# Kernel optimization log

Hardware: AMD Instinct MI355X
Metric: run time of the kernel (lower is better)

Reference implementation:

```python
import jax, jax.numpy as jnp
import numpy as np

D_MODEL = 1024


def setup_inputs() -> dict:
    key = jax.random.key(0)
    kx, kq, kk, kv = jax.random.split(key, 4)
    x = jax.random.normal(kx, (4, 2048, D_MODEL), dtype=jnp.float32)
    s = 1.0 / np.sqrt(D_MODEL)
    # torch nn.Linear weight is [out, in]; y = x @ W.T
    Wq = jax.random.normal(kq, (D_MODEL, D_MODEL), dtype=jnp.float32) * s
    Wk = jax.random.normal(kk, (D_MODEL, D_MODEL), dtype=jnp.float32) * s
    Wv = jax.random.normal(kv, (D_MODEL, D_MODEL), dtype=jnp.float32) * s
    return {"x": x, "Wq": Wq, "Wk": Wk, "Wv": Wv}


def reference(x, Wq, Wk, Wv):
    # Linear projections (no bias): [b, s, d]
    Q = jnp.einsum("bsd,ed->bse", x, Wq)
    K = jnp.einsum("bsd,ed->bse", x, Wk)
    V = jnp.einsum("bsd,ed->bse", x, Wv)
    d_k = Q.shape[-1]
    scores = jnp.einsum("bqd,bkd->bqk", Q, K) / jnp.sqrt(jnp.asarray(d_k, Q.dtype))
    weights = jax.nn.softmax(scores, axis=-1)
    return jnp.einsum("bqk,bkd->bqd", weights, V)
```

## Files before the change

### kernel.cpp

```cpp
#include <hip/hip_runtime.h>
#include <hip/hip_bf16.h>

using bf16 = __hip_bfloat16;
typedef __attribute__((ext_vector_type(8))) short short8;
typedef __attribute__((ext_vector_type(16))) float f32x16;

__global__ __launch_bounds__(256) void cast_all(const float* __restrict__ x,
                                                const float* __restrict__ Wq,
                                                const float* __restrict__ Wk,
                                                const float* __restrict__ Wv,
                                                bf16* __restrict__ xb, bf16* __restrict__ Wb) {
  const int r0 = blockIdx.x << 2;
  const float* src;
  bf16* dst;
  if (r0 < 8192) {
    src = x + (size_t)r0 * 1024;
    dst = xb + (size_t)r0 * 1024;
  } else if (r0 < 9216) {
    src = Wq + (size_t)(r0 - 8192) * 1024;
    dst = Wb + (size_t)(r0 - 8192) * 1024;
  } else if (r0 < 10240) {
    src = Wk + (size_t)(r0 - 9216) * 1024;
    dst = Wb + (size_t)(r0 - 8192) * 1024;
  } else {
    src = Wv + (size_t)(r0 - 10240) * 1024;
    dst = Wb + (size_t)(r0 - 8192) * 1024;
  }
  const int i = threadIdx.x * 16;
#pragma unroll
  for (int q = 0; q < 4; ++q) {
    const float4 f = *(const float4*)(src + i + q * 4);
    bf16 h[4];
    h[0] = __float2bfloat16(f.x);
    h[1] = __float2bfloat16(f.y);
    h[2] = __float2bfloat16(f.z);
    h[3] = __float2bfloat16(f.w);
    *(uint2*)(dst + i + q * 4) = *(const uint2*)h;
  }
}

template <int BN, class Epi>
__device__ __forceinline__ void gemm_nt(const bf16* __restrict__ A, const bf16* __restrict__ B,
                                        int lda, int ldb, int K, int m0, int n0, Epi epi) {
  constexpr int THREADS = BN * 2;
  constexpr int NA = 8192 / (THREADS * 16);
  constexpr int NB = (BN * 64) / (THREADS * 16);
  constexpr int L = NA + NB;
  constexpr int SLOT = (128 + BN) * 64;
  __shared__ char smem[3 * SLOT];
  const int t = threadIdx.x;
  const int lane = t & 63;
  const int wave = t >> 6;
  const int wm = (BN == 256) ? (wave >> 2) * 64 : (wave >> 1) * 64;
  const int wn = (BN == 256) ? (wave & 3) * 64 : (wave & 1) * 64;
  const int rl = lane & 31;
  const int grp = lane >> 5;

  f32x16 acc[2][2];
#pragma unroll
  for (int i = 0; i < 2; ++i)
#pragma unroll
    for (int j = 0; j < 2; ++j)
#pragma unroll
      for (int r = 0; r < 16; ++r) acc[i][j][r] = 0.f;

  const bf16* gA[NA];
#pragma unroll
  for (int j = 0; j < NA; ++j) {
    const int s = j * THREADS + t;
    const int row = s >> 2;
    const int f = (row + (row >> 2)) & 3;
    gA[j] = A + (size_t)(m0 + row) * lda + ((((s & 3) ^ f)) << 3);
  }
  const bf16* gB[NB];
#pragma unroll
  for (int j = 0; j < NB; ++j) {
    const int s = j * THREADS + t;
    const int row = s >> 2;
    const int f = (row + (row >> 2)) & 3;
    gB[j] = B + (size_t)(n0 + row) * ldb + ((((s & 3) ^ f)) << 3);
  }

  auto stage = [&](int kt, int slot) {
    char* base = smem + slot * SLOT;
    bf16* As = (bf16*)base;
    bf16* Bs = (bf16*)(base + 8192);
    const int k0 = kt * 32;
#pragma unroll
    for (int j = 0; j < NA; ++j)
      __builtin_amdgcn_global_load_lds(
          (const __attribute__((address_space(1))) unsigned int*)(gA[j] + k0),
          (__attribute__((address_space(3))) unsigned int*)(As + (j * THREADS + wave * 64) * 8),
          16, 0, 0);
#pragma unroll
    for (int j = 0; j < NB; ++j)
      __builtin_amdgcn_global_load_lds(
          (const __attribute__((address_space(1))) unsigned int*)(gB[j] + k0),
          (__attribute__((address_space(3))) unsigned int*)(Bs + (j * THREADS + wave * 64) * 8),
          16, 0, 0);
  };

  const int NT = K >> 5;

  stage(0, 0);
  stage(1, 1);
  if constexpr (BN == 256) {
    asm volatile("s_waitcnt vmcnt(3)" ::: "memory");
  } else {
    asm volatile("s_waitcnt vmcnt(4)" ::: "memory");
  }
  __builtin_amdgcn_s_barrier();
  __builtin_amdgcn_sched_barrier(0);

  int s0 = 0;
  for (int kt = 0; kt < NT; ++kt) {
    const int s1 = (s0 == 2) ? 0 : s0 + 1;
    const int s2 = (s1 == 2) ? 0 : s1 + 1;
    const char* base = smem + s0 * SLOT;
    const bf16* As = (const bf16*)base;
    const bf16* Bs = (const bf16*)(base + 8192);

    if (kt + 2 < NT) stage(kt + 2, s2);

    short8 af[2][2], bv[2][2];
#pragma unroll
    for (int ks = 0; ks < 2; ++ks) {
      const int kb = ks * 2 + grp;
#pragma unroll
      for (int mt = 0; mt < 2; ++mt) {
        const int rowa = wm + mt * 32 + rl;
        const int fa = (rowa + (rowa >> 2)) & 3;
        af[ks][mt] = *(const short8*)(As + rowa * 32 + ((kb ^ fa) << 3));
        const int rowb = wn + mt * 32 + rl;
        const int fb = (rowb + (rowb >> 2)) & 3;
        bv[ks][mt] = *(const short8*)(Bs + rowb * 32 + ((kb ^ fb) << 3));
      }
    }
    __builtin_amdgcn_sched_barrier(0);
    asm volatile("s_waitcnt lgkmcnt(0)" ::: "memory");
    __builtin_amdgcn_sched_barrier(0);
    __builtin_amdgcn_s_setprio(1);
#pragma unroll
    for (int ks = 0; ks < 2; ++ks)
#pragma unroll
      for (int mt = 0; mt < 2; ++mt)
#pragma unroll
        for (int nt = 0; nt < 2; ++nt)
          acc[mt][nt] = __builtin_amdgcn_mfma_f32_32x32x16_bf16(af[ks][mt], bv[ks][nt],
                                                                acc[mt][nt], 0, 0, 0);
    __builtin_amdgcn_s_setprio(0);
    __builtin_amdgcn_sched_barrier(0);
    if (kt + 1 < NT) {
      if (kt + 2 < NT) {
        if constexpr (BN == 256) {
          asm volatile("s_waitcnt vmcnt(3)" ::: "memory");
        } else {
          asm volatile("s_waitcnt vmcnt(4)" ::: "memory");
        }
      } else {
        asm volatile("s_waitcnt vmcnt(0)" ::: "memory");
      }
      __builtin_amdgcn_s_barrier();
      __builtin_amdgcn_sched_barrier(0);
    }
    s0 = s1;
  }
  __syncthreads();

  epi(acc, m0, n0, wm, wn, lane, wave, smem);
}

__device__ __forceinline__ int c_row(int reg, int lane) {
  return (reg & 3) + 8 * (reg >> 2) + 4 * (lane >> 5);
}

template <class F>
__device__ __forceinline__ void for_each_c(const f32x16 (&acc)[2][2], int wm, int wn, int lane,
                                           F f) {
  const int rl = lane & 31;
#pragma unroll
  for (int mt = 0; mt < 2; ++mt)
#pragma unroll
    for (int nt = 0; nt < 2; ++nt)
#pragma unroll
      for (int reg = 0; reg < 16; ++reg)
        f(wm + mt * 32 + c_row(reg, lane), wn + nt * 32 + rl, acc[mt][nt][reg]);
}

__global__ __launch_bounds__(512, 4) void proj_kernel(const bf16* __restrict__ xb,
                                                      const bf16* __restrict__ Wb,
                                                      bf16* __restrict__ Qb,
                                                      bf16* __restrict__ Kb,
                                                      bf16* __restrict__ Vt) {
  const int id = blockIdx.y * 12 + blockIdx.x;
  const int g = id & 7, s = id >> 3;
  const int m0 = (g * 8 + (s & 7)) * 128;
  const int n0 = (s >> 3) * 256;
  gemm_nt<256>(xb, Wb, 1024, 1024, 1024, m0, n0,
          [=](const f32x16 (&acc)[2][2], int m0, int n0, int wm, int wn, int lane, int wave,
              char* smem) {
    if (n0 < 2048) {
      bf16* dst = (n0 < 1024) ? Qb : Kb;
      const int nb = (n0 < 1024) ? n0 : (n0 - 1024);
      for_each_c(acc, wm, wn, lane, [&](int m, int n, float v) {
        dst[(size_t)(m0 + m) * 1024 + nb + n] = __float2bfloat16(v);
      });
    } else {
      bf16* T = (bf16*)(smem) + wave * 2304;
      const int rl = lane & 31;
      const int g4 = 4 * (lane >> 5);
      const int mbase = m0 + wm;
      const int bb = mbase >> 11;
      const int sbase = mbase & 2047;
      const int nvbase = n0 - 2048 + wn;
#pragma unroll
      for (int p = 0; p < 2; ++p) {
#pragma unroll
        for (int mt = 0; mt < 2; ++mt)
#pragma unroll
          for (int q = 0; q < 4; ++q) {
            bf16 h4[4];
#pragma unroll
            for (int r = 0; r < 4; ++r) h4[r] = __float2bfloat16(acc[mt][p][4 * q + r]);
            *(uint2*)(T + rl * 72 + mt * 32 + 8 * q + g4) = *(const uint2*)h4;
          }
        asm volatile("s_waitcnt lgkmcnt(0)" ::: "memory");
#pragma unroll
        for (int i = 0; i < 4; ++i) {
          const int nl = i * 8 + (lane >> 3);
          const int ml = (lane & 7) * 8;
          const short8 val = *(const short8*)(T + nl * 72 + ml);
          *(short8*)(Vt + ((size_t)bb * 1024 + nvbase + p * 32 + nl) * 2048 + sbase + ml) = val;
        }
        asm volatile("s_waitcnt lgkmcnt(0)" ::: "memory");
      }
    }
  });
}

__global__ __launch_bounds__(512, 4) void qk_exp_kernel(const bf16* __restrict__ Qb,
                                                        const bf16* __restrict__ Kb,
                                                        bf16* __restrict__ E,
                                                        float* __restrict__ Lpart) {
  const int z = blockIdx.y;
  const int id2 = blockIdx.x;
  const int g = id2 & 7, s = id2 >> 3;
  const int m0 = ((g & 3) * 4 + (s & 3)) * 128;
  const int n0 = ((g >> 2) * 4 + (s >> 2)) * 256;
  const bf16* A = Qb + (size_t)z * 2048 * 1024;
  const bf16* B = Kb + (size_t)z * 2048 * 1024;
  bf16* Ez = E + (size_t)z * 2048 * 2048;
  float* Lz = Lpart + (size_t)z * 8 * 2048;
  gemm_nt<256>(A, B, 1024, 1024, 1024, m0, n0,
          [=](const f32x16 (&acc)[2][2], int m0, int n0, int wm, int wn, int lane, int wave,
              char* smem) {
    float* Lp = (float*)smem;
    const int rl = lane & 31;
#pragma unroll
    for (int mt = 0; mt < 2; ++mt)
#pragma unroll
      for (int reg = 0; reg < 16; ++reg) {
        const int mr = wm + mt * 32 + c_row(reg, lane);
        float s2 = 0.f;
#pragma unroll
        for (int nt = 0; nt < 2; ++nt) {
          const float e = __expf(acc[mt][nt][reg] * 0.03125f);
          Ez[(size_t)(m0 + mr) * 2048 + n0 + wn + nt * 32 + rl] = __float2bfloat16(e);
          s2 += e;
        }
        s2 += __shfl_xor(s2, 1, 64);
        s2 += __shfl_xor(s2, 2, 64);
        s2 += __shfl_xor(s2, 4, 64);
        s2 += __shfl_xor(s2, 8, 64);
        s2 += __shfl_xor(s2, 16, 64);
        if (rl == 0) Lp[mr * 4 + (wave & 3)] = s2;
      }
    __syncthreads();
    const int t = threadIdx.x;
    if (t < 128)
      Lz[(n0 >> 8) * 2048 + m0 + t] =
          Lp[t * 4 + 0] + Lp[t * 4 + 1] + Lp[t * 4 + 2] + Lp[t * 4 + 3];
  });
}

__global__ __launch_bounds__(256, 4) void pv_kernel(const bf16* __restrict__ E,
                                                    const bf16* __restrict__ Vt,
                                                    const float* __restrict__ Lpart,
                                                    float* __restrict__ out) {
  const int z = blockIdx.y;
  const int id2 = blockIdx.x;
  const int g = id2 & 7, s = id2 >> 3;
  const int m0 = ((g & 3) * 4 + (s & 3)) * 128;
  const int n0 = ((g >> 2) * 4 + (s >> 2)) * 128;
  const bf16* A = E + (size_t)z * 2048 * 2048;
  const bf16* B = Vt + (size_t)z * 1024 * 2048;
  const float* Lz = Lpart + (size_t)z * 8 * 2048;
  float* oz = out + (size_t)z * 2048 * 1024;
  gemm_nt<128>(A, B, 2048, 2048, 2048, m0, n0,
          [=](const f32x16 (&acc)[2][2], int m0, int n0, int wm, int wn, int lane, int wave,
              char* smem) {
    float* Lsm = (float*)smem;
    const int t = threadIdx.x;
    if (t < 128) {
      float s2 = 0.f;
#pragma unroll
      for (int i = 0; i < 8; ++i) s2 += Lz[(size_t)i * 2048 + m0 + t];
      Lsm[t] = 1.f / s2;
    }
    __syncthreads();
    const int rl = lane & 31;
#pragma unroll
    for (int mt = 0; mt < 2; ++mt)
#pragma unroll
      for (int reg = 0; reg < 16; ++reg) {
        const int ml = wm + mt * 32 + c_row(reg, lane);
        const float il = Lsm[ml];
#pragma unroll
        for (int nt = 0; nt < 2; ++nt)
          oz[(size_t)(m0 + ml) * 1024 + n0 + wn + nt * 32 + rl] = acc[mt][nt][reg] * il;
      }
  });
}

extern "C" void kernel_launch(void* const* d_in, const int* in_sizes, int n_in,
                              void* d_out, int out_size, void* d_ws, size_t ws_size,
                              hipStream_t stream) {
  const float* x = (const float*)d_in[0];
  const float* Wq = (const float*)d_in[1];
  const float* Wk = (const float*)d_in[2];
  const float* Wv = (const float*)d_in[3];
  float* out = (float*)d_out;

  char* w = (char*)d_ws;
  bf16* xb = (bf16*)w; w += (size_t)8192 * 1024 * 2;
  bf16* Wb = (bf16*)w; w += (size_t)3072 * 1024 * 2;
  bf16* Qb = (bf16*)w; w += (size_t)8192 * 1024 * 2;
  bf16* Kb = (bf16*)w; w += (size_t)8192 * 1024 * 2;
  bf16* Vt = (bf16*)w; w += (size_t)8192 * 1024 * 2;
  bf16* E  = (bf16*)w; w += (size_t)4 * 2048 * 2048 * 2;
  float* Lpart = (float*)w; w += (size_t)4 * 8 * 2048 * 4;

  cast_all<<<2816, 256, 0, stream>>>(x, Wq, Wk, Wv, xb, Wb);

  proj_kernel<<<dim3(12, 64), 512, 0, stream>>>(xb, Wb, Qb, Kb, Vt);

  qk_exp_kernel<<<dim3(128, 4), 512, 0, stream>>>(Qb, Kb, E, Lpart);

  pv_kernel<<<dim3(128, 4), 256, 0, stream>>>(E, Vt, Lpart, out);
}
```

Baseline: 235.7 us.

## Enlarge PV GEMM tiles, relax LDS wait placement, simplify cast kernel

The PV GEMM now uses 128x256 tiles with 512 threads and half as many blocks, raising per-block reuse of the E and V tiles. The GEMM main loop drops the explicit LDS wait and scheduling barriers before the MFMAs and folds lgkmcnt(0) into the end-of-iteration wait, letting the compiler overlap LDS reads with MFMAs. The cast kernel is changed to one row per block with four floats per thread. The larger tiles lower occupancy and leave one block per CU, which may hurt latency hiding.

```diff
diff --git a/kernel.cpp b/kernel.cpp
--- a/kernel.cpp
+++ b/kernel.cpp
@@ -10,33 +10,30 @@
                                                 const float* __restrict__ Wk,
                                                 const float* __restrict__ Wv,
                                                 bf16* __restrict__ xb, bf16* __restrict__ Wb) {
-  const int r0 = blockIdx.x << 2;
+  const int b = blockIdx.x;
   const float* src;
   bf16* dst;
-  if (r0 < 8192) {
-    src = x + (size_t)r0 * 1024;
-    dst = xb + (size_t)r0 * 1024;
-  } else if (r0 < 9216) {
-    src = Wq + (size_t)(r0 - 8192) * 1024;
-    dst = Wb + (size_t)(r0 - 8192) * 1024;
-  } else if (r0 < 10240) {
-    src = Wk + (size_t)(r0 - 9216) * 1024;
-    dst = Wb + (size_t)(r0 - 8192) * 1024;
+  if (b < 8192) {
+    src = x + (size_t)b * 1024;
+    dst = xb + (size_t)b * 1024;
+  } else if (b < 9216) {
+    src = Wq + (size_t)(b - 8192) * 1024;
+    dst = Wb + (size_t)(b - 8192) * 1024;
+  } else if (b < 10240) {
+    src = Wk + (size_t)(b - 9216) * 1024;
+    dst = Wb + (size_t)(b - 8192) * 1024;
   } else {
-    src = Wv + (size_t)(r0 - 10240) * 1024;
-    dst = Wb + (size_t)(r0 - 8192) * 1024;
-  }
-  const int i = threadIdx.x * 16;
-#pragma unroll
-  for (int q = 0; q < 4; ++q) {
-    const float4 f = *(const float4*)(src + i + q * 4);
-    bf16 h[4];
-    h[0] = __float2bfloat16(f.x);
-    h[1] = __float2bfloat16(f.y);
-    h[2] = __float2bfloat16(f.z);
-    h[3] = __float2bfloat16(f.w);
-    *(uint2*)(dst + i + q * 4) = *(const uint2*)h;
-  }
+    src = Wv + (size_t)(b - 10240) * 1024;
+    dst = Wb + (size_t)(b - 8192) * 1024;
+  }
+  const int i = threadIdx.x * 4;
+  const float4 f = *(const float4*)(src + i);
+  bf16 h[4];
+  h[0] = __float2bfloat16(f.x);
+  h[1] = __float2bfloat16(f.y);
+  h[2] = __float2bfloat16(f.z);
+  h[3] = __float2bfloat16(f.w);
+  *(uint2*)(dst + i) = *(const uint2*)h;
 }
 
 template <int BN, class Epi>
@@ -104,7 +101,7 @@
 
   stage(0, 0);
   stage(1, 1);
-  if constexpr (BN == 256) {
+  if constexpr (L == 3) {
     asm volatile("s_waitcnt vmcnt(3)" ::: "memory");
   } else {
     asm volatile("s_waitcnt vmcnt(4)" ::: "memory");
@@ -136,9 +133,6 @@
         bv[ks][mt] = *(const short8*)(Bs + rowb * 32 + ((kb ^ fb) << 3));
       }
     }
-    __builtin_amdgcn_sched_barrier(0);
-    asm volatile("s_waitcnt lgkmcnt(0)" ::: "memory");
-    __builtin_amdgcn_sched_barrier(0);
     __builtin_amdgcn_s_setprio(1);
 #pragma unroll
     for (int ks = 0; ks < 2; ++ks)
@@ -149,16 +143,15 @@
           acc[mt][nt] = __builtin_amdgcn_mfma_f32_32x32x16_bf16(af[ks][mt], bv[ks][nt],
                                                                 acc[mt][nt], 0, 0, 0);
     __builtin_amdgcn_s_setprio(0);
-    __builtin_amdgcn_sched_barrier(0);
     if (kt + 1 < NT) {
       if (kt + 2 < NT) {
-        if constexpr (BN == 256) {
-          asm volatile("s_waitcnt vmcnt(3)" ::: "memory");
+        if constexpr (L == 3) {
+          asm volatile("s_waitcnt vmcnt(3) lgkmcnt(0)" ::: "memory");
         } else {
-          asm volatile("s_waitcnt vmcnt(4)" ::: "memory");
+          asm volatile("s_waitcnt vmcnt(4) lgkmcnt(0)" ::: "memory");
         }
       } else {
-        asm volatile("s_waitcnt vmcnt(0)" ::: "memory");
+        asm volatile("s_waitcnt vmcnt(0) lgkmcnt(0)" ::: "memory");
       }
       __builtin_amdgcn_s_barrier();
       __builtin_amdgcn_sched_barrier(0);
@@ -283,7 +276,7 @@
   });
 }
 
-__global__ __launch_bounds__(256, 4) void pv_kernel(const bf16* __restrict__ E,
+__global__ __launch_bounds__(512, 4) void pv_kernel(const bf16* __restrict__ E,
                                                     const bf16* __restrict__ Vt,
                                                     const float* __restrict__ Lpart,
                                                     float* __restrict__ out) {
@@ -291,12 +284,12 @@
   const int id2 = blockIdx.x;
   const int g = id2 & 7, s = id2 >> 3;
   const int m0 = ((g & 3) * 4 + (s & 3)) * 128;
-  const int n0 = ((g >> 2) * 4 + (s >> 2)) * 128;
+  const int n0 = ((g >> 2) * 2 + (s >> 2)) * 256;
   const bf16* A = E + (size_t)z * 2048 * 2048;
   const bf16* B = Vt + (size_t)z * 1024 * 2048;
   const float* Lz = Lpart + (size_t)z * 8 * 2048;
   float* oz = out + (size_t)z * 2048 * 1024;
-  gemm_nt<128>(A, B, 2048, 2048, 2048, m0, n0,
+  gemm_nt<256>(A, B, 2048, 2048, 2048, m0, n0,
           [=](const f32x16 (&acc)[2][2], int m0, int n0, int wm, int wn, int lane, int wave,
               char* smem) {
     float* Lsm = (float*)smem;
@@ -340,11 +333,11 @@
   bf16* E  = (bf16*)w; w += (size_t)4 * 2048 * 2048 * 2;
   float* Lpart = (float*)w; w += (size_t)4 * 8 * 2048 * 4;
 
-  cast_all<<<2816, 256, 0, stream>>>(x, Wq, Wk, Wv, xb, Wb);
+  cast_all<<<11264, 256, 0, stream>>>(x, Wq, Wk, Wv, xb, Wb);
 
   proj_kernel<<<dim3(12, 64), 512, 0, stream>>>(xb, Wb, Qb, Kb, Vt);
 
   qk_exp_kernel<<<dim3(128, 4), 512, 0, stream>>>(Qb, Kb, E, Lpart);
 
-  pv_kernel<<<dim3(128, 4), 256, 0, stream>>>(E, Vt, Lpart, out);
-}
+  pv_kernel<<<dim3(64, 4), 512, 0, stream>>>(E, Vt, Lpart, out);
+}
```

Measured after the change: 229.2 us. 2.8% less time.
